# Optimization experiments

Measured on AMD Instinct MI355X. Metric: run time of the kernel, lower is better.

## Reference

```python
import jax, jax.numpy as jnp
import numpy as np

IN_DIM = 128
OUT_DIM = 64
ALPHA = 0.2  # LeakyReLU negative slope


def _xavier(key, shape):
    # matches nn.init.xavier_uniform_ with gain=1.414
    fan_in, fan_out = shape
    limit = 1.414 * np.sqrt(6.0 / (fan_in + fan_out))
    return jax.random.uniform(key, shape, jnp.float32, -limit, limit)


def setup_inputs() -> dict:
    key = jax.random.key(0)
    ks = jax.random.split(key, 12)
    N_C, N_P, N_I, E = 200000, 200000, 100000, 1000000
    return {
        "taxPayer_feats": jax.random.normal(ks[0], (N_C, IN_DIM), jnp.float32),
        "person_feats": jax.random.normal(ks[1], (N_P, IN_DIM), jnp.float32),
        "item_feats": jax.random.normal(ks[2], (N_I, IN_DIM), jnp.float32),
        "idx_c0": jax.random.randint(ks[3], (E,), 0, N_C, jnp.int64 if jax.config.jax_enable_x64 else jnp.int32),
        "idx_c1": jax.random.randint(ks[4], (E,), 0, N_C, jnp.int64 if jax.config.jax_enable_x64 else jnp.int32),
        "idx_p": jax.random.randint(ks[5], (E,), 0, N_P, jnp.int64 if jax.config.jax_enable_x64 else jnp.int32),
        "P_company": _xavier(ks[6], (IN_DIM, OUT_DIM)),
        "P_person": _xavier(ks[7], (IN_DIM, OUT_DIM)),
        "P_item": _xavier(ks[8], (IN_DIM, OUT_DIM)),
        "W_PCC": _xavier(ks[9], (OUT_DIM * 3, OUT_DIM)),
    }


def reference(taxPayer_feats, person_feats, item_feats, idx_c0, idx_c1, idx_p,
              P_company, P_person, P_item, W_PCC):
    # InstanceAggLayer.forward, pattern_name='PCC'
    f_taxPayer = taxPayer_feats @ P_company   # [N_C, D]
    f_person = person_feats @ P_person        # [N_P, D]
    f_item = item_feats @ P_item              # computed in original (unused for PCC)
    d = f_taxPayer.shape[1]
    # cat([f_c[i0], f_c[i1], f_p[i2]], dim=1) @ W_PCC  ==  sum of slice matmuls
    # (same math, avoids materializing the [E, 3D] concat)
    pre = (f_taxPayer[idx_c0] @ W_PCC[:d]
           + f_taxPayer[idx_c1] @ W_PCC[d:2 * d]
           + f_person[idx_p] @ W_PCC[2 * d:])
    instance = jnp.where(pre >= 0, pre, ALPHA * pre)  # LeakyReLU
    return instance
```

## Files before the change

kernel.cpp:

```cpp
#include <hip/hip_runtime.h>

#define IN_DIM 128
#define OUT_DIM 64
#define ALPHA 0.2f

typedef __attribute__((ext_vector_type(8))) short short8v;
typedef __attribute__((ext_vector_type(4))) float f32x4;
typedef __attribute__((ext_vector_type(4))) unsigned int u32x4;

__device__ __forceinline__ unsigned short bf16rne(float x) {
    union { float f; unsigned u; } c; c.f = x;
    const unsigned u = c.u;
    return (unsigned short)((u + 0x7fffu + ((u >> 16) & 1u)) >> 16);
}

__global__ __launch_bounds__(256) void compute_M_kernel(
    const float* __restrict__ P_company,
    const float* __restrict__ P_person,
    const float* __restrict__ W_PCC,
    float* __restrict__ M,
    unsigned short* __restrict__ Mt)
{
    const int mb = blockIdx.x >> 4;
    const int chunk = blockIdx.x & 15;
    const float* __restrict__ P = (mb == 2) ? P_person : P_company;
    const float* __restrict__ Wb = W_PCC + mb * OUT_DIM * OUT_DIM;
    float* __restrict__ Mb = M + mb * IN_DIM * OUT_DIM;
    const int base = chunk * 512;
    for (int idx = base + threadIdx.x; idx < base + 512; idx += 256) {
        const int r = idx >> 6;
        const int c = idx & 63;
        float acc = 0.f;
#pragma unroll
        for (int k = 0; k < OUT_DIM; ++k)
            acc = fmaf(P[r * OUT_DIM + k], Wb[k * OUT_DIM + c], acc);
        Mb[idx] = acc;
        Mt[(mb * OUT_DIM + c) * IN_DIM + r] = bf16rne(acc);
    }
}

union F4 { float4 v; float f[4]; };

__device__ __forceinline__ void load_X(F4* L, const float* __restrict__ feats,
                                       int nrows, int tile, int fr, int fq) {
    long long ar = (long long)tile * 16 + fr;
    if (ar >= nrows) ar = nrows - 1;
    const float* __restrict__ A = feats + ar * IN_DIM;
#pragma unroll
    for (int k0i = 0; k0i < 4; ++k0i) {
        L[k0i * 2 + 0].v = *(const float4*)(A + k0i * 32 + fq * 4);
        L[k0i * 2 + 1].v = *(const float4*)(A + k0i * 32 + 16 + fq * 4);
    }
}

__device__ __forceinline__ void table_body(
    const float* __restrict__ feats, int nrows,
    const unsigned short* __restrict__ Mtb,
    unsigned short* __restrict__ out,
    int tile0, int tstride)
{
    const int lane = threadIdx.x & 63;
    const int fr   = lane & 15;
    const int fq   = lane >> 4;

    union FragU { short8v v; uint2 q[2]; };
    short8v mfrag[4][4];
#pragma unroll
    for (int k0i = 0; k0i < 4; ++k0i)
#pragma unroll
        for (int c0i = 0; c0i < 4; ++c0i) {
            const unsigned short* p =
                Mtb + ((size_t)(c0i * 16 + fr)) * IN_DIM + k0i * 32 + fq * 4;
            FragU f;
            f.q[0] = *(const uint2*)(p);
            f.q[1] = *(const uint2*)(p + 16);
            mfrag[k0i][c0i] = f.v;
        }

    const int ntiles = (nrows + 15) >> 4;
    union AF { short8v v; unsigned short u[8]; };

    int tile = tile0;
    if (tile >= ntiles) return;
    F4 La[8];
    load_X(La, feats, nrows, tile, fr, fq);

    for (; tile < ntiles; tile += tstride) {
        const int next = tile + tstride;
        F4 Lb[8];
        if (next < ntiles) load_X(Lb, feats, nrows, next, fr, fq);

        short8v xfrag[4];
#pragma unroll
        for (int k0i = 0; k0i < 4; ++k0i) {
            AF af;
#pragma unroll
            for (int j = 0; j < 4; ++j) {
                af.u[j]     = bf16rne(La[k0i * 2 + 0].f[j]);
                af.u[4 + j] = bf16rne(La[k0i * 2 + 1].f[j]);
            }
            xfrag[k0i] = af.v;
        }

        f32x4 acc[4];
#pragma unroll
        for (int c0i = 0; c0i < 4; ++c0i) acc[c0i] = (f32x4){0.f, 0.f, 0.f, 0.f};
#pragma unroll
        for (int k0i = 0; k0i < 4; ++k0i)
#pragma unroll
            for (int c0i = 0; c0i < 4; ++c0i)
                acc[c0i] = __builtin_amdgcn_mfma_f32_16x16x32_bf16(
                    mfrag[k0i][c0i], xfrag[k0i], acc[c0i], 0, 0, 0);

        const long long gr = (long long)tile * 16 + fr;
        if (gr < nrows) {
            unsigned short* __restrict__ orow = out + gr * OUT_DIM + fq * 4;
#pragma unroll
            for (int c0i = 0; c0i < 4; ++c0i) {
                union { unsigned short s[4]; uint2 q; } pk;
#pragma unroll
                for (int j = 0; j < 4; ++j) pk.s[j] = bf16rne(acc[c0i][j]);
                *(uint2*)(orow + c0i * 16) = pk.q;
            }
        }

#pragma unroll
        for (int i = 0; i < 8; ++i) La[i] = Lb[i];
    }
}

__global__ __launch_bounds__(256) void tables_kernel(
    const float* __restrict__ T, int n_c,
    const float* __restrict__ Pp, int n_p,
    const unsigned short* __restrict__ Mt,
    unsigned short* __restrict__ g0,
    unsigned short* __restrict__ g2,
    int gsplit)
{
    const int w = threadIdx.x >> 6;
    if ((int)blockIdx.x < gsplit) {
        const int table = w & 1;
        const int tile0 = (int)blockIdx.x * 2 + (w >> 1);
        table_body(T, n_c,
                   Mt + (size_t)table * OUT_DIM * IN_DIM,
                   g0 + (size_t)table * n_c * OUT_DIM,
                   tile0, gsplit * 2);
    } else {
        const int bid = (int)blockIdx.x - gsplit;
        const int nb  = (int)gridDim.x - gsplit;
        table_body(Pp, n_p,
                   Mt + (size_t)2 * OUT_DIM * IN_DIM,
                   g2, bid * 4 + w, nb * 4);
    }
}

__global__ __launch_bounds__(256) void gather_kernel(
    const int* __restrict__ i0, const int* __restrict__ i1, const int* __restrict__ i2,
    const unsigned short* __restrict__ g0, const unsigned short* __restrict__ g1,
    const unsigned short* __restrict__ g2,
    float* __restrict__ out, long long E)
{
    const long long t = (long long)blockIdx.x * 256 + threadIdx.x;
    const long long grp = t >> 3;
    const int j = (int)t & 7;
    const long long e0 = grp * 4;
    if (e0 >= E) return;

    long long e[4];
    bool live[4];
#pragma unroll
    for (int k = 0; k < 4; ++k) {
        e[k] = e0 + k;
        live[k] = e[k] < E;
        if (!live[k]) e[k] = E - 1;
    }

    int a0[4], a1[4], a2[4];
#pragma unroll
    for (int k = 0; k < 4; ++k) {
        a0[k] = i0[e[k]];
        a1[k] = i1[e[k]];
        a2[k] = i2[e[k]];
    }

    u32x4 v0[4], v1[4], v2[4];
#pragma unroll
    for (int k = 0; k < 4; ++k) {
        v0[k] = *(const u32x4*)(g0 + (long long)a0[k] * OUT_DIM + j * 8);
        v1[k] = *(const u32x4*)(g1 + (long long)a1[k] * OUT_DIM + j * 8);
        v2[k] = *(const u32x4*)(g2 + (long long)a2[k] * OUT_DIM + j * 8);
    }

#pragma unroll
    for (int k = 0; k < 4; ++k) {
        float s[8];
#pragma unroll
        for (int m = 0; m < 4; ++m) {
            const unsigned u0 = v0[k][m], u1 = v1[k][m], u2 = v2[k][m];
            const float lo = __uint_as_float(u0 << 16)
                           + __uint_as_float(u1 << 16)
                           + __uint_as_float(u2 << 16);
            const float hi = __uint_as_float(u0 & 0xffff0000u)
                           + __uint_as_float(u1 & 0xffff0000u)
                           + __uint_as_float(u2 & 0xffff0000u);
            s[2 * m]     = lo >= 0.f ? lo : ALPHA * lo;
            s[2 * m + 1] = hi >= 0.f ? hi : ALPHA * hi;
        }
        if (live[k]) {
            float* __restrict__ o = out + e[k] * OUT_DIM + j * 8;
            const f32x4 q0 = {s[0], s[1], s[2], s[3]};
            const f32x4 q1 = {s[4], s[5], s[6], s[7]};
            __builtin_nontemporal_store(q0, (f32x4*)(o));
            __builtin_nontemporal_store(q1, (f32x4*)(o + 4));
        }
    }
}

__global__ __launch_bounds__(256) void fused_fallback_kernel(
    const float* __restrict__ T, const float* __restrict__ Pp,
    const int* __restrict__ i0, const int* __restrict__ i1, const int* __restrict__ i2,
    const float* __restrict__ M, float* __restrict__ out, long long E)
{
    const int wave = threadIdx.x >> 6;
    const int lane = threadIdx.x & 63;
    const long long wavesTotal = (long long)gridDim.x * 4;
    const float* __restrict__ M0 = M;
    const float* __restrict__ M1 = M + IN_DIM * OUT_DIM;
    const float* __restrict__ M2 = M + 2 * IN_DIM * OUT_DIM;
    for (long long e = (long long)blockIdx.x * 4 + wave; e < E; e += wavesTotal) {
        const float* __restrict__ x0 = T + (long long)i0[e] * IN_DIM;
        const float* __restrict__ x1 = T + (long long)i1[e] * IN_DIM;
        const float* __restrict__ x2 = Pp + (long long)i2[e] * IN_DIM;
        float acc = 0.f;
#pragma unroll 4
        for (int k = 0; k < IN_DIM; ++k) {
            acc = fmaf(x0[k], M0[k * OUT_DIM + lane], acc);
            acc = fmaf(x1[k], M1[k * OUT_DIM + lane], acc);
            acc = fmaf(x2[k], M2[k * OUT_DIM + lane], acc);
        }
        acc = acc >= 0.f ? acc : ALPHA * acc;
        out[e * OUT_DIM + lane] = acc;
    }
}

extern "C" void kernel_launch(void* const* d_in, const int* in_sizes, int n_in,
                              void* d_out, int out_size, void* d_ws, size_t ws_size,
                              hipStream_t stream) {
    const float* T    = (const float*)d_in[0];
    const float* Pp   = (const float*)d_in[1];
    const int*   i0   = (const int*)d_in[3];
    const int*   i1   = (const int*)d_in[4];
    const int*   i2   = (const int*)d_in[5];
    const float* Pc   = (const float*)d_in[6];
    const float* Pper = (const float*)d_in[7];
    const float* W    = (const float*)d_in[9];
    float* out = (float*)d_out;

    const int n_c = in_sizes[0] / IN_DIM;
    const int n_p = in_sizes[1] / IN_DIM;
    const long long E = in_sizes[3];

    float* M = (float*)d_ws;
    unsigned short* Mt = (unsigned short*)((char*)d_ws + 98304);
    const size_t tblOff = 98304 + 49152;
    const size_t tblBytes = ((size_t)n_c * 2 + (size_t)n_p) * OUT_DIM * sizeof(unsigned short);

    compute_M_kernel<<<48, 256, 0, stream>>>(Pc, Pper, W, M, Mt);

    if (ws_size >= tblOff + tblBytes) {
        unsigned short* g0 = (unsigned short*)((char*)d_ws + tblOff);
        unsigned short* g1 = g0 + (size_t)n_c * OUT_DIM;
        unsigned short* g2 = g1 + (size_t)n_c * OUT_DIM;

        const int GA = 1024;
        const int GB = 512;
        tables_kernel<<<GA + GB, 256, 0, stream>>>(T, n_c, Pp, n_p, Mt, g0, g2, GA);

        const long long groups = (E + 3) / 4;
        const long long threads = groups * 8;
        gather_kernel<<<(int)((threads + 255) / 256), 256, 0, stream>>>(
            i0, i1, i2, g0, g1, g2, out, E);
    } else {
        fused_fallback_kernel<<<16384, 256, 0, stream>>>(T, Pp, i0, i1, i2, M, out, E);
    }
}
```

Measured before the change: 191.4 us.

## Stage feature rows through LDS as bf16 in tables kernel with coalesced loads

The tables kernel now loads 64-row super-tiles of input features with fully coalesced float4 loads, converts them to bf16 once, and stores them in shared memory. MFMA input fragments are then read from LDS, so the two company-table waves share one global read of each row instead of each wave loading it separately. The per-wave register double-buffered prefetch is dropped in favour of block-level synchronisation, which can expose load latency. The person-table block count is raised to rebalance work.

```diff
diff --git a/kernel.cpp b/kernel.cpp
--- a/kernel.cpp
+++ b/kernel.cpp
@@ -3,6 +3,8 @@
 #define IN_DIM 128
 #define OUT_DIM 64
 #define ALPHA 0.2f
+#define SROWS 64
+#define LROW 132
 
 typedef __attribute__((ext_vector_type(8))) short short8v;
 typedef __attribute__((ext_vector_type(4))) float f32x4;
@@ -39,29 +41,29 @@
     }
 }
 
-union F4 { float4 v; float f[4]; };
-
-__device__ __forceinline__ void load_X(F4* L, const float* __restrict__ feats,
-                                       int nrows, int tile, int fr, int fq) {
-    long long ar = (long long)tile * 16 + fr;
-    if (ar >= nrows) ar = nrows - 1;
-    const float* __restrict__ A = feats + ar * IN_DIM;
-#pragma unroll
-    for (int k0i = 0; k0i < 4; ++k0i) {
-        L[k0i * 2 + 0].v = *(const float4*)(A + k0i * 32 + fq * 4);
-        L[k0i * 2 + 1].v = *(const float4*)(A + k0i * 32 + 16 + fq * 4);
-    }
-}
-
-__device__ __forceinline__ void table_body(
-    const float* __restrict__ feats, int nrows,
-    const unsigned short* __restrict__ Mtb,
-    unsigned short* __restrict__ out,
-    int tile0, int tstride)
-{
+__global__ __launch_bounds__(256) void tables_kernel(
+    const float* __restrict__ T, int n_c,
+    const float* __restrict__ Pp, int n_p,
+    const unsigned short* __restrict__ Mt,
+    unsigned short* __restrict__ g0,
+    unsigned short* __restrict__ g2,
+    int gsplit)
+{
+    __shared__ unsigned short xs[SROWS][LROW];
+    const int w    = threadIdx.x >> 6;
     const int lane = threadIdx.x & 63;
     const int fr   = lane & 15;
     const int fq   = lane >> 4;
+
+    const bool isC = (int)blockIdx.x < gsplit;
+    const float* __restrict__ feats = isC ? T : Pp;
+    const int nrows = isC ? n_c : n_p;
+    const int bid   = isC ? (int)blockIdx.x : (int)blockIdx.x - gsplit;
+    const int nb    = isC ? gsplit : (int)gridDim.x - gsplit;
+    const int table = isC ? (w & 1) : 2;
+    unsigned short* __restrict__ outp =
+        isC ? g0 + (size_t)(w & 1) * n_c * OUT_DIM : g2;
+    const unsigned short* __restrict__ Mtb = Mt + (size_t)table * OUT_DIM * IN_DIM;
 
     union FragU { short8v v; uint2 q[2]; };
     short8v mfrag[4][4];
@@ -77,80 +79,61 @@
             mfrag[k0i][c0i] = f.v;
         }
 
-    const int ntiles = (nrows + 15) >> 4;
-    union AF { short8v v; unsigned short u[8]; };
-
-    int tile = tile0;
-    if (tile >= ntiles) return;
-    F4 La[8];
-    load_X(La, feats, nrows, tile, fr, fq);
-
-    for (; tile < ntiles; tile += tstride) {
-        const int next = tile + tstride;
-        F4 Lb[8];
-        if (next < ntiles) load_X(Lb, feats, nrows, next, fr, fq);
-
-        short8v xfrag[4];
-#pragma unroll
-        for (int k0i = 0; k0i < 4; ++k0i) {
-            AF af;
-#pragma unroll
-            for (int j = 0; j < 4; ++j) {
-                af.u[j]     = bf16rne(La[k0i * 2 + 0].f[j]);
-                af.u[4 + j] = bf16rne(La[k0i * 2 + 1].f[j]);
+    const int nsup = (nrows + SROWS - 1) / SROWS;
+    for (int sup = bid; sup < nsup; sup += nb) {
+        const long long row0 = (long long)sup * SROWS;
+        __syncthreads();
+#pragma unroll
+        for (int it = 0; it < (SROWS * (IN_DIM / 4)) / 256; ++it) {
+            const int i  = it * 256 + threadIdx.x;
+            const int r  = i >> 5;
+            const int c4 = i & 31;
+            long long gr = row0 + r;
+            if (gr >= nrows) gr = nrows - 1;
+            const float4 v = *(const float4*)(feats + gr * IN_DIM + c4 * 4);
+            union { unsigned short s[4]; uint2 q; } b;
+            b.s[0] = bf16rne(v.x); b.s[1] = bf16rne(v.y);
+            b.s[2] = bf16rne(v.z); b.s[3] = bf16rne(v.w);
+            *(uint2*)&xs[r][c4 * 4] = b.q;
+        }
+        __syncthreads();
+
+        const int nt = isC ? 2 : 1;
+#pragma unroll
+        for (int ti = 0; ti < 2; ++ti) {
+            if (ti >= nt) break;
+            const int lr = isC ? ((w >> 1) * 32 + ti * 16) : (w * 16);
+            short8v xfrag[4];
+#pragma unroll
+            for (int k0i = 0; k0i < 4; ++k0i) {
+                FragU af;
+                af.q[0] = *(const uint2*)&xs[lr + fr][k0i * 32 + fq * 4];
+                af.q[1] = *(const uint2*)&xs[lr + fr][k0i * 32 + 16 + fq * 4];
+                xfrag[k0i] = af.v;
             }
-            xfrag[k0i] = af.v;
-        }
-
-        f32x4 acc[4];
-#pragma unroll
-        for (int c0i = 0; c0i < 4; ++c0i) acc[c0i] = (f32x4){0.f, 0.f, 0.f, 0.f};
-#pragma unroll
-        for (int k0i = 0; k0i < 4; ++k0i)
-#pragma unroll
-            for (int c0i = 0; c0i < 4; ++c0i)
-                acc[c0i] = __builtin_amdgcn_mfma_f32_16x16x32_bf16(
-                    mfrag[k0i][c0i], xfrag[k0i], acc[c0i], 0, 0, 0);
-
-        const long long gr = (long long)tile * 16 + fr;
-        if (gr < nrows) {
-            unsigned short* __restrict__ orow = out + gr * OUT_DIM + fq * 4;
-#pragma unroll
-            for (int c0i = 0; c0i < 4; ++c0i) {
-                union { unsigned short s[4]; uint2 q; } pk;
-#pragma unroll
-                for (int j = 0; j < 4; ++j) pk.s[j] = bf16rne(acc[c0i][j]);
-                *(uint2*)(orow + c0i * 16) = pk.q;
+
+            f32x4 acc[4];
+#pragma unroll
+            for (int c0i = 0; c0i < 4; ++c0i) acc[c0i] = (f32x4){0.f, 0.f, 0.f, 0.f};
+#pragma unroll
+            for (int k0i = 0; k0i < 4; ++k0i)
+#pragma unroll
+                for (int c0i = 0; c0i < 4; ++c0i)
+                    acc[c0i] = __builtin_amdgcn_mfma_f32_16x16x32_bf16(
+                        mfrag[k0i][c0i], xfrag[k0i], acc[c0i], 0, 0, 0);
+
+            const long long gr = row0 + lr + fr;
+            if (gr < nrows) {
+                unsigned short* __restrict__ orow = outp + gr * OUT_DIM + fq * 4;
+#pragma unroll
+                for (int c0i = 0; c0i < 4; ++c0i) {
+                    union { unsigned short s[4]; uint2 q; } pk;
+#pragma unroll
+                    for (int j = 0; j < 4; ++j) pk.s[j] = bf16rne(acc[c0i][j]);
+                    *(uint2*)(orow + c0i * 16) = pk.q;
+                }
             }
         }
-
-#pragma unroll
-        for (int i = 0; i < 8; ++i) La[i] = Lb[i];
-    }
-}
-
-__global__ __launch_bounds__(256) void tables_kernel(
-    const float* __restrict__ T, int n_c,
-    const float* __restrict__ Pp, int n_p,
-    const unsigned short* __restrict__ Mt,
-    unsigned short* __restrict__ g0,
-    unsigned short* __restrict__ g2,
-    int gsplit)
-{
-    const int w = threadIdx.x >> 6;
-    if ((int)blockIdx.x < gsplit) {
-        const int table = w & 1;
-        const int tile0 = (int)blockIdx.x * 2 + (w >> 1);
-        table_body(T, n_c,
-                   Mt + (size_t)table * OUT_DIM * IN_DIM,
-                   g0 + (size_t)table * n_c * OUT_DIM,
-                   tile0, gsplit * 2);
-    } else {
-        const int bid = (int)blockIdx.x - gsplit;
-        const int nb  = (int)gridDim.x - gsplit;
-        table_body(Pp, n_p,
-                   Mt + (size_t)2 * OUT_DIM * IN_DIM,
-                   g2, bid * 4 + w, nb * 4);
     }
 }
 
@@ -273,7 +256,7 @@
         unsigned short* g2 = g1 + (size_t)n_c * OUT_DIM;
 
         const int GA = 1024;
-        const int GB = 512;
+        const int GB = 768;
         tables_kernel<<<GA + GB, 256, 0, stream>>>(T, n_c, Pp, n_p, Mt, g0, g2, GA);
 
         const long long groups = (E + 3) / 4;
```

Result: slower. 206.7 us (+8.0%).

## Compute both company tables per X tile and split table kernels

Applied to the files above, without the earlier changes.

The company feature matrix was previously read twice, once per W slice, by separate waves. Now each wave loads one X tile and runs MFMAs against both projection matrices, writing g0 and g1 together, which halves reads of the 200000x128 fp32 input. The person table moves into its own kernel launch. The trade-off is higher register pressure from two fragment sets and accumulators, and the two tables now run in sequence instead of concurrently in one grid.

```diff
diff --git a/kernel.cpp b/kernel.cpp
--- a/kernel.cpp
+++ b/kernel.cpp
@@ -53,17 +53,108 @@
     }
 }
 
-__device__ __forceinline__ void table_body(
-    const float* __restrict__ feats, int nrows,
-    const unsigned short* __restrict__ Mtb,
-    unsigned short* __restrict__ out,
-    int tile0, int tstride)
-{
+union FragU { short8v v; uint2 q[2]; };
+union AF { short8v v; unsigned short u[8]; };
+
+__global__ __launch_bounds__(256, 2) void tablesC_kernel(
+    const float* __restrict__ T, int n_c,
+    const unsigned short* __restrict__ Mt,
+    unsigned short* __restrict__ g0,
+    unsigned short* __restrict__ g1)
+{
+    const int w    = threadIdx.x >> 6;
     const int lane = threadIdx.x & 63;
     const int fr   = lane & 15;
     const int fq   = lane >> 4;
 
-    union FragU { short8v v; uint2 q[2]; };
+    short8v mfrag[2][4][4];
+#pragma unroll
+    for (int t = 0; t < 2; ++t)
+#pragma unroll
+        for (int k0i = 0; k0i < 4; ++k0i)
+#pragma unroll
+            for (int c0i = 0; c0i < 4; ++c0i) {
+                const unsigned short* p = Mt + (size_t)t * OUT_DIM * IN_DIM +
+                    ((size_t)(c0i * 16 + fr)) * IN_DIM + k0i * 32 + fq * 4;
+                FragU f;
+                f.q[0] = *(const uint2*)(p);
+                f.q[1] = *(const uint2*)(p + 16);
+                mfrag[t][k0i][c0i] = f.v;
+            }
+
+    const int ntiles  = (n_c + 15) >> 4;
+    const int wstride = gridDim.x * 4;
+    int tile = (int)blockIdx.x * 4 + w;
+    if (tile >= ntiles) return;
+
+    F4 La[8];
+    load_X(La, T, n_c, tile, fr, fq);
+
+    for (; tile < ntiles; tile += wstride) {
+        const int next = tile + wstride;
+        F4 Lb[8];
+        if (next < ntiles) load_X(Lb, T, n_c, next, fr, fq);
+
+        short8v xfrag[4];
+#pragma unroll
+        for (int k0i = 0; k0i < 4; ++k0i) {
+            AF af;
+#pragma unroll
+            for (int j = 0; j < 4; ++j) {
+                af.u[j]     = bf16rne(La[k0i * 2 + 0].f[j]);
+                af.u[4 + j] = bf16rne(La[k0i * 2 + 1].f[j]);
+            }
+            xfrag[k0i] = af.v;
+        }
+
+        f32x4 acc0[4], acc1[4];
+#pragma unroll
+        for (int c0i = 0; c0i < 4; ++c0i) {
+            acc0[c0i] = (f32x4){0.f, 0.f, 0.f, 0.f};
+            acc1[c0i] = (f32x4){0.f, 0.f, 0.f, 0.f};
+        }
+#pragma unroll
+        for (int k0i = 0; k0i < 4; ++k0i)
+#pragma unroll
+            for (int c0i = 0; c0i < 4; ++c0i) {
+                acc0[c0i] = __builtin_amdgcn_mfma_f32_16x16x32_bf16(
+                    mfrag[0][k0i][c0i], xfrag[k0i], acc0[c0i], 0, 0, 0);
+                acc1[c0i] = __builtin_amdgcn_mfma_f32_16x16x32_bf16(
+                    mfrag[1][k0i][c0i], xfrag[k0i], acc1[c0i], 0, 0, 0);
+            }
+
+        const long long gr = (long long)tile * 16 + fr;
+        if (gr < n_c) {
+            unsigned short* __restrict__ o0 = g0 + gr * OUT_DIM + fq * 4;
+            unsigned short* __restrict__ o1 = g1 + gr * OUT_DIM + fq * 4;
+#pragma unroll
+            for (int c0i = 0; c0i < 4; ++c0i) {
+                union { unsigned short s[4]; uint2 q; } p0, p1;
+#pragma unroll
+                for (int j = 0; j < 4; ++j) {
+                    p0.s[j] = bf16rne(acc0[c0i][j]);
+                    p1.s[j] = bf16rne(acc1[c0i][j]);
+                }
+                *(uint2*)(o0 + c0i * 16) = p0.q;
+                *(uint2*)(o1 + c0i * 16) = p1.q;
+            }
+        }
+
+#pragma unroll
+        for (int i = 0; i < 8; ++i) La[i] = Lb[i];
+    }
+}
+
+__global__ __launch_bounds__(256) void tablesP_kernel(
+    const float* __restrict__ Pp, int n_p,
+    const unsigned short* __restrict__ Mtb,
+    unsigned short* __restrict__ g2)
+{
+    const int w    = threadIdx.x >> 6;
+    const int lane = threadIdx.x & 63;
+    const int fr   = lane & 15;
+    const int fq   = lane >> 4;
+
     short8v mfrag[4][4];
 #pragma unroll
     for (int k0i = 0; k0i < 4; ++k0i)
@@ -77,18 +168,18 @@
             mfrag[k0i][c0i] = f.v;
         }
 
-    const int ntiles = (nrows + 15) >> 4;
-    union AF { short8v v; unsigned short u[8]; };
-
-    int tile = tile0;
+    const int ntiles  = (n_p + 15) >> 4;
+    const int wstride = gridDim.x * 4;
+    int tile = (int)blockIdx.x * 4 + w;
     if (tile >= ntiles) return;
+
     F4 La[8];
-    load_X(La, feats, nrows, tile, fr, fq);
-
-    for (; tile < ntiles; tile += tstride) {
-        const int next = tile + tstride;
+    load_X(La, Pp, n_p, tile, fr, fq);
+
+    for (; tile < ntiles; tile += wstride) {
+        const int next = tile + wstride;
         F4 Lb[8];
-        if (next < ntiles) load_X(Lb, feats, nrows, next, fr, fq);
+        if (next < ntiles) load_X(Lb, Pp, n_p, next, fr, fq);
 
         short8v xfrag[4];
 #pragma unroll
@@ -113,8 +204,8 @@
                     mfrag[k0i][c0i], xfrag[k0i], acc[c0i], 0, 0, 0);
 
         const long long gr = (long long)tile * 16 + fr;
-        if (gr < nrows) {
-            unsigned short* __restrict__ orow = out + gr * OUT_DIM + fq * 4;
+        if (gr < n_p) {
+            unsigned short* __restrict__ orow = g2 + gr * OUT_DIM + fq * 4;
 #pragma unroll
             for (int c0i = 0; c0i < 4; ++c0i) {
                 union { unsigned short s[4]; uint2 q; } pk;
@@ -126,31 +217,6 @@
 
 #pragma unroll
         for (int i = 0; i < 8; ++i) La[i] = Lb[i];
-    }
-}
-
-__global__ __launch_bounds__(256) void tables_kernel(
-    const float* __restrict__ T, int n_c,
-    const float* __restrict__ Pp, int n_p,
-    const unsigned short* __restrict__ Mt,
-    unsigned short* __restrict__ g0,
-    unsigned short* __restrict__ g2,
-    int gsplit)
-{
-    const int w = threadIdx.x >> 6;
-    if ((int)blockIdx.x < gsplit) {
-        const int table = w & 1;
-        const int tile0 = (int)blockIdx.x * 2 + (w >> 1);
-        table_body(T, n_c,
-                   Mt + (size_t)table * OUT_DIM * IN_DIM,
-                   g0 + (size_t)table * n_c * OUT_DIM,
-                   tile0, gsplit * 2);
-    } else {
-        const int bid = (int)blockIdx.x - gsplit;
-        const int nb  = (int)gridDim.x - gsplit;
-        table_body(Pp, n_p,
-                   Mt + (size_t)2 * OUT_DIM * IN_DIM,
-                   g2, bid * 4 + w, nb * 4);
     }
 }
 
@@ -272,9 +338,9 @@
         unsigned short* g1 = g0 + (size_t)n_c * OUT_DIM;
         unsigned short* g2 = g1 + (size_t)n_c * OUT_DIM;
 
-        const int GA = 1024;
-        const int GB = 512;
-        tables_kernel<<<GA + GB, 256, 0, stream>>>(T, n_c, Pp, n_p, Mt, g0, g2, GA);
+        tablesC_kernel<<<1024, 256, 0, stream>>>(T, n_c, Mt, g0, g1);
+        tablesP_kernel<<<512, 256, 0, stream>>>(
+            Pp, n_p, Mt + (size_t)2 * OUT_DIM * IN_DIM, g2);
 
         const long long groups = (E + 3) / 4;
         const long long threads = groups * 8;
```

Measured after the change: 195.5 us. 1.02x slower.
